# Kernel optimization log

Measured on AMD Instinct MI355X. Metric: run time of the kernel, lower is better.

The kernel has to match this reference:

```python
import jax, jax.numpy as jnp
import numpy as np

HEADS, DK, DV = 8, 64, 64
DM = HEADS * DK                 # 512
ROUNDS, SEQ, BUCKET = 2, 4096, 64
NCHUNK = SEQ // BUCKET          # 64 chunks
NBUCKETS = SEQ // BUCKET        # 64 hash buckets (Reformer convention)
SCALE = 8.0                     # sqrt(d_k)
NEG_BIG = -1e15
BATCH = 4


def setup_inputs() -> dict:
    key = jax.random.key(0)
    kq, kk, kv, kr = jax.random.split(key, 4)
    q = jax.random.normal(kq, (BATCH, SEQ, DM), jnp.float32)
    k = jax.random.normal(kk, (BATCH, SEQ, DM), jnp.float32)
    v = jax.random.normal(kv, (BATCH, SEQ, DM), jnp.float32)
    # angular-LSH random rotations: (rounds, d_model, n_buckets//2)
    R = jax.random.normal(kr, (ROUNDS, DM, NBUCKETS // 2), jnp.float32)
    return {"q": q, "k": k, "v": v, "R": R}


def _window(x):
    # x: (r, b, S, ...) -> (r, b, n_chunks, 2*BUCKET, ...)
    # each window = [previous chunk (wrapped), current chunk]
    r, b, S = x.shape[:3]
    xc = x.reshape((r, b, NCHUNK, BUCKET) + x.shape[3:])
    return jnp.concatenate([jnp.roll(xc, 1, axis=2), xc], axis=3)


def _lsh_attention(q, k, v, R):
    b = q.shape[0]
    # --- hash queries (same sorted_idx reused for q, k, v, as in the module) ---
    rot = jnp.einsum('bsd,rdm->rbsm', q, R)                       # (r,b,S,nb/2)
    h = jnp.argmax(jnp.concatenate([rot, -rot], axis=-1), axis=-1)
    h = h.astype(jnp.int32) + 1                                    # bucket 0 reserved for padding
    sorted_idx = jnp.argsort(h, axis=-1, stable=True)              # (r,b,S)

    def gather(x):  # (b,S,d) -> (r,b,S,d) sorted by bucket per round
        xb = jnp.broadcast_to(x[None], (ROUNDS,) + x.shape)
        return jnp.take_along_axis(xb, sorted_idx[..., None], axis=2)

    qs, ks, vs = gather(q), gather(k), gather(v)
    hs = jnp.take_along_axis(h, sorted_idx, axis=2)                # (r,b,S)

    # --- chunk into local windows ---
    qs = _window(qs.reshape(ROUNDS, b, SEQ, HEADS, DK))            # (r,b,n,2c,h,dk)
    ks = _window(ks.reshape(ROUNDS, b, SEQ, HEADS, DK))
    vs = _window(vs.reshape(ROUNDS, b, SEQ, HEADS, DV))
    hw = _window(hs)                                               # (r,b,n,2c)

    # --- per-window attention with bucket mask + log-count bias ---
    attn = jnp.einsum('rbnqhd,rbnkhd->rbnhqk', qs, ks) / SCALE     # (r,b,n,h,2c,2c)
    hm = (hw[:, :, :, :, None] == hw[:, :, :, None, :]) & (hw[:, :, :, :, None] != 0)
    hm = hm[:, :, :, None].astype(jnp.float32)                     # (r,b,n,1,2c,2c)
    cnt = hm * jnp.sum(hm, axis=4, keepdims=True)                  # count term (sum over q dim, as in source)
    bias = (1.0 - hm) * NEG_BIG - jnp.log(jnp.clip(cnt, 1.0))
    attn = attn + bias
    attn = attn + jnp.eye(2 * BUCKET, dtype=attn.dtype) * -1e5     # self-attention mask
    attn = jax.nn.softmax(attn, axis=-1)
    out = jnp.einsum('rbnhml,rbnlhd->rbnmhd', attn, vs)            # (r,b,n,2c,h,dv)
    out = out[:, :, :, BUCKET:]                                    # keep current-chunk queries
    out = out.reshape(ROUNDS, b, SEQ, HEADS, DV)

    # --- unsort back to original token order, sum over rounds ---
    inv = jnp.argsort(sorted_idx, axis=-1, stable=True)
    out = jnp.take_along_axis(out, inv[:, :, :, None, None], axis=2)
    return jnp.sum(out, axis=0)                                    # (b,S,heads,dv)


def reference(q, k, v, R):
    return _lsh_attention(q, k, v, R)
```

## Files before the change

### kernel.cpp

```cpp
#include <hip/hip_runtime.h>
#include <hip/hip_bf16.h>
#include <hip/hip_fp16.h>

#define HEADS 8
#define DK 64
#define DV 64
#define DM 512
#define ROUNDS 2
#define SEQ 4096
#define BUCKET 64
#define NCHUNK 64
#define BATCH 4
#define GAP_THRESH 0.02f

typedef _Float16 f16;
typedef f16 f16x4 __attribute__((ext_vector_type(4)));
typedef f16 f16x8 __attribute__((ext_vector_type(8)));
typedef float f32x4 __attribute__((ext_vector_type(4)));

#define MFMA16(a, b, c) __builtin_amdgcn_mfma_f32_16x16x32_f16((a), (b), (c), 0, 0, 0)

__global__ __launch_bounds__(256) void hash_approx_kernel(
    const float* __restrict__ q, const float* __restrict__ R,
    int* __restrict__ h_out, unsigned char* __restrict__ flag) {
  int blk = blockIdx.x;
  int stile = blk & 63;
  int b = (blk >> 6) & (BATCH - 1);
  int r = blk >> 8;
  int s0 = stile << 6;
  int rb = r * BATCH + b;

  __shared__ f16 Rh[32 * 520];
  __shared__ f16 Rl[32 * 520];

  int tid = threadIdx.x;
  int w = tid >> 6, lane = tid & 63, lo = lane & 15, hi = lane >> 4;

  const float* rbase = R + (size_t)r * DM * 32;
#pragma unroll
  for (int i = 0; i < 16; ++i) {
    int fi = tid + i * 256;
    float4 rv = *reinterpret_cast<const float4*>(rbase + fi * 4);
    int d = fi >> 3, m0 = (fi & 7) * 4;
    const float* rp = &rv.x;
#pragma unroll
    for (int e = 0; e < 4; ++e) {
      float x = rp[e];
      f16 hx = (f16)x;
      Rh[(m0 + e) * 520 + d] = hx;
      Rl[(m0 + e) * 520 + d] = (f16)(x - (float)hx);
    }
  }
  __syncthreads();

  int qr = w * 16 + lo;
  const float* qp = q + ((size_t)b * SEQ + s0 + qr) * DM;

  f32x4 acc0 = {0.f, 0.f, 0.f, 0.f}, acc1 = {0.f, 0.f, 0.f, 0.f};
#pragma unroll 4
  for (int ks = 0; ks < 16; ++ks) {
    int k = ks * 32 + hi * 8;
    float4 a0 = *reinterpret_cast<const float4*>(qp + k);
    float4 a1 = *reinterpret_cast<const float4*>(qp + k + 4);
    float av[8] = {a0.x, a0.y, a0.z, a0.w, a1.x, a1.y, a1.z, a1.w};
    f16x8 ahi, alo;
#pragma unroll
    for (int e = 0; e < 8; ++e) {
      f16 hx = (f16)av[e];
      ahi[e] = hx;
      alo[e] = (f16)(av[e] - (float)hx);
    }
    f16x8 bh0 = *reinterpret_cast<const f16x8*>(&Rh[lo * 520 + k]);
    f16x8 bl0 = *reinterpret_cast<const f16x8*>(&Rl[lo * 520 + k]);
    f16x8 bh1 = *reinterpret_cast<const f16x8*>(&Rh[(16 + lo) * 520 + k]);
    f16x8 bl1 = *reinterpret_cast<const f16x8*>(&Rl[(16 + lo) * 520 + k]);
    acc0 = MFMA16(ahi, bh0, acc0);
    acc0 = MFMA16(ahi, bl0, acc0);
    acc0 = MFMA16(alo, bh0, acc0);
    acc1 = MFMA16(ahi, bh1, acc1);
    acc1 = MFMA16(ahi, bl1, acc1);
    acc1 = MFMA16(alo, bh1, acc1);
  }

#pragma unroll
  for (int rg = 0; rg < 4; ++rg) {
    float c0 = acc0[rg], c1 = acc1[rg];
    float v1 = c0;
    int i1 = lo;
    float v2 = -INFINITY;
    float cv[3] = {c1, -c0, -c1};
    int ci[3] = {16 + lo, 32 + lo, 48 + lo};
#pragma unroll
    for (int c = 0; c < 3; ++c) {
      if (cv[c] > v1) { v2 = v1; v1 = cv[c]; i1 = ci[c]; }
      else v2 = fmaxf(v2, cv[c]);
    }
#pragma unroll
    for (int off = 1; off <= 8; off <<= 1) {
      float ov1 = __shfl_xor(v1, off);
      int oi1 = __shfl_xor(i1, off);
      float ov2 = __shfl_xor(v2, off);
      if (ov1 > v1 || (ov1 == v1 && oi1 < i1)) {
        v2 = fmaxf(v1, ov2);
        v1 = ov1;
        i1 = oi1;
      } else {
        v2 = fmaxf(v2, ov1);
      }
    }
    if (lo == 0) {
      int grow = s0 + w * 16 + hi * 4 + rg;
      size_t gid = (size_t)rb * SEQ + grow;
      h_out[gid] = i1 + 1;
      flag[gid] = (v1 - v2 <= GAP_THRESH) ? 1 : 0;
    }
  }
}

__global__ __launch_bounds__(256) void hash_exact_kernel(
    const float* __restrict__ q, const float* __restrict__ R,
    const unsigned char* __restrict__ flag, int* __restrict__ h_out) {
  int g0 = blockIdx.x * 64;
  __shared__ int nf;
  __shared__ unsigned char list[64];
  __shared__ double pl[8][33];
  int tid = threadIdx.x;
  if (tid == 0) nf = 0;
  __syncthreads();
  if (tid < 64 && flag[g0 + tid]) {
    int idx = atomicAdd(&nf, 1);
    list[idx] = (unsigned char)tid;
  }
  __syncthreads();
  int n = nf;
  for (int i = 0; i < n; ++i) {
    int g = g0 + list[i];
    int rb = g >> 12, s = g & (SEQ - 1);
    int r = rb >> 2, b = rb & (BATCH - 1);
    int m = tid & 31, chunk = tid >> 5;
    const float* qp = q + ((size_t)b * SEQ + s) * DM;
    const float* rp = R + (size_t)r * DM * 32;
    double part = 0.0;
    for (int dd = 0; dd < 64; ++dd) {
      int d = chunk * 64 + dd;
      part = fma((double)qp[d], (double)rp[(size_t)d * 32 + m], part);
    }
    pl[chunk][m] = part;
    __syncthreads();
    if (tid < 32) {
      double sum = 0.0;
#pragma unroll
      for (int c = 0; c < 8; ++c) sum += pl[c][m];
      double v = sum;
      int ix = m;
      double nv = -sum;
      if (nv > v) { v = nv; ix = m + 32; }
      for (int off = 1; off <= 16; off <<= 1) {
        double ov = __shfl_xor(v, off);
        int oi = __shfl_xor(ix, off);
        if (ov > v || (ov == v && oi < ix)) { v = ov; ix = oi; }
      }
      if (tid == 0) h_out[g] = ix + 1;
    }
    __syncthreads();
  }
}

__global__ __launch_bounds__(256) void sort_kernel(const int* __restrict__ h,
                                                   int* __restrict__ sorted_idx) {
  int rb = blockIdx.x;
  const int* hp = h + (size_t)rb * SEQ;
  __shared__ unsigned char hs[SEQ];
  __shared__ unsigned char rs[SEQ];
  __shared__ int tile_cnt[64][64];
  __shared__ int tile_base[64][64];
  __shared__ int bucket_base[64];
  __shared__ int bucket_tot[64];
  int tid = threadIdx.x;
  int wave = tid >> 6, lane = tid & 63;
  for (int i = tid; i < 64 * 64; i += 256) ((int*)tile_cnt)[i] = 0;
  __syncthreads();
  for (int t = wave; t < 64; t += 4) {
    int s = (t << 6) + lane;
    int hv = hp[s] - 1;
    unsigned long long mm = ~0ull;
#pragma unroll
    for (int bit = 0; bit < 6; ++bit) {
      unsigned long long bb = __ballot((hv >> bit) & 1);
      mm &= ((hv >> bit) & 1) ? bb : ~bb;
    }
    int rank = __popcll(mm & ((1ull << lane) - 1ull));
    hs[s] = (unsigned char)hv;
    rs[s] = (unsigned char)rank;
    if (rank == 0) tile_cnt[t][hv] = __popcll(mm);
  }
  __syncthreads();
  if (tid < 64) {
    int bkt = tid;
    int run = 0;
    for (int t = 0; t < 64; ++t) { tile_base[t][bkt] = run; run += tile_cnt[t][bkt]; }
    bucket_tot[bkt] = run;
  }
  __syncthreads();
  if (tid == 0) {
    int run = 0;
    for (int bkt = 0; bkt < 64; ++bkt) { bucket_base[bkt] = run; run += bucket_tot[bkt]; }
  }
  __syncthreads();
  for (int t = wave; t < 64; t += 4) {
    int s = (t << 6) + lane;
    int hv = hs[s];
    int pos = bucket_base[hv] + tile_base[t][hv] + rs[s];
    sorted_idx[(size_t)rb * SEQ + pos] = s;
  }
}

__global__ __launch_bounds__(256, 4) void attn_kernel(
    const float* __restrict__ q, const float* __restrict__ k,
    const float* __restrict__ v, const int* __restrict__ h,
    const int* __restrict__ sidx, float* __restrict__ out) {
  int x = blockIdx.x;
  int hd = x & 7;
  int n = (x >> 3) & 63;
  int b = (x >> 9) & (BATCH - 1);
  int r = x >> 11;
  int rb = r * BATCH + b;

  __shared__ __align__(16) unsigned char smem[34816];
  __shared__ int orig_w[128];
  __shared__ int hw[128];
  f16* Qh = reinterpret_cast<f16*>(smem);
  f16* Kh = reinterpret_cast<f16*>(smem + 9216);
  const int VOFF = 17408;

  int tid = threadIdx.x;
  int wave = tid >> 6;
  int lane = tid & 63;
  int lo = lane & 15;
  int hi = lane >> 4;

  if (tid < 128) {
    int j = tid;
    int sp = (j < 64) ? ((((n + 63) & 63) << 6) + j) : ((n << 6) + (j - 64));
    int orig = sidx[(size_t)rb * SEQ + sp];
    orig_w[j] = orig;
    hw[j] = h[(size_t)rb * SEQ + orig];
  }
  __syncthreads();

  const size_t gbase = (size_t)b * SEQ * DM + hd * 64;

  float4 kreg[8], qreg[4];
#pragma unroll
  for (int t = 0; t < 8; ++t) {
    int idx = tid + t * 256;
    int j = idx >> 4, dq = idx & 15;
    kreg[t] = *reinterpret_cast<const float4*>(
        k + gbase + (size_t)orig_w[j] * DM + dq * 4);
  }
#pragma unroll
  for (int t = 0; t < 4; ++t) {
    int idx = tid + t * 256;
    int i = idx >> 4, dq = idx & 15;
    qreg[t] = *reinterpret_cast<const float4*>(
        q + gbase + (size_t)orig_w[64 + i] * DM + dq * 4);
  }
#pragma unroll
  for (int t = 0; t < 8; ++t) {
    int idx = tid + t * 256;
    int j = idx >> 4, dq = idx & 15;
    f16x4 hv = {(f16)kreg[t].x, (f16)kreg[t].y, (f16)kreg[t].z, (f16)kreg[t].w};
    *reinterpret_cast<f16x4*>(&Kh[j * 72 + dq * 4]) = hv;
  }
#pragma unroll
  for (int t = 0; t < 4; ++t) {
    int idx = tid + t * 256;
    int i = idx >> 4, dq = idx & 15;
    f16x4 hv = {(f16)qreg[t].x, (f16)qreg[t].y, (f16)qreg[t].z, (f16)qreg[t].w};
    *reinterpret_cast<f16x4*>(&Qh[i * 72 + dq * 4]) = hv;
  }
  __syncthreads();

  float4 vreg[8];
#pragma unroll
  for (int t = 0; t < 8; ++t) {
    int idx = tid + t * 256;
    int l = idx >> 4, dq = idx & 15;
    vreg[t] = *reinterpret_cast<const float4*>(
        v + gbase + (size_t)orig_w[l] * DM + dq * 4);
  }

  f32x4 acc[8];
#pragma unroll
  for (int t = 0; t < 8; ++t) acc[t] = (f32x4){0.f, 0.f, 0.f, 0.f};

  int qr_a = wave * 16 + lo;
  f16x8 aq0 = *reinterpret_cast<const f16x8*>(&Qh[qr_a * 72 + hi * 8]);
  f16x8 aq1 = *reinterpret_cast<const f16x8*>(&Qh[qr_a * 72 + 32 + hi * 8]);
#pragma unroll
  for (int t = 0; t < 8; ++t) {
    f16x8 b0 = *reinterpret_cast<const f16x8*>(&Kh[(t * 16 + lo) * 72 + hi * 8]);
    f16x8 b1 = *reinterpret_cast<const f16x8*>(&Kh[(t * 16 + lo) * 72 + 32 + hi * 8]);
    acc[t] = MFMA16(aq0, b0, acc[t]);
    acc[t] = MFMA16(aq1, b1, acc[t]);
  }

  int hq[4];
#pragma unroll
  for (int rg = 0; rg < 4; ++rg) hq[rg] = hw[64 + wave * 16 + hi * 4 + rg];
#pragma unroll
  for (int t = 0; t < 8; ++t) {
    int key = t * 16 + lo;
    int hj = hw[key];
#pragma unroll
    for (int rg = 0; rg < 4; ++rg) {
      int qr = wave * 16 + hi * 4 + rg;
      float lg = acc[t][rg] * 0.125f;
      if (hj != hq[rg]) lg = -1e15f;
      if (key == 64 + qr) lg -= 1e5f;
      acc[t][rg] = lg;
    }
  }
  float mx[4] = {-INFINITY, -INFINITY, -INFINITY, -INFINITY};
#pragma unroll
  for (int t = 0; t < 8; ++t)
#pragma unroll
    for (int rg = 0; rg < 4; ++rg) mx[rg] = fmaxf(mx[rg], acc[t][rg]);
#pragma unroll
  for (int off = 1; off <= 8; off <<= 1)
#pragma unroll
    for (int rg = 0; rg < 4; ++rg) mx[rg] = fmaxf(mx[rg], __shfl_xor(mx[rg], off));
  float sm[4] = {0.f, 0.f, 0.f, 0.f};
#pragma unroll
  for (int t = 0; t < 8; ++t)
#pragma unroll
    for (int rg = 0; rg < 4; ++rg) {
      float ev = __expf(acc[t][rg] - mx[rg]);
      acc[t][rg] = ev;
      sm[rg] += ev;
    }
#pragma unroll
  for (int off = 1; off <= 8; off <<= 1)
#pragma unroll
    for (int rg = 0; rg < 4; ++rg) sm[rg] += __shfl_xor(sm[rg], off);
  float inv[4];
#pragma unroll
  for (int rg = 0; rg < 4; ++rg) inv[rg] = 1.0f / sm[rg];

  __syncthreads();

#pragma unroll
  for (int t = 0; t < 8; ++t) {
    int key = t * 16 + lo;
#pragma unroll
    for (int rg = 0; rg < 4; ++rg) {
      int qr = wave * 16 + hi * 4 + rg;
      *reinterpret_cast<f16*>(smem + qr * 272 + key * 2) =
          (f16)(acc[t][rg] * inv[rg]);
    }
  }
#pragma unroll
  for (int t = 0; t < 8; ++t) {
    int idx = tid + t * 256;
    int l = idx >> 4, dq = idx & 15;
    const float* vp = &vreg[t].x;
#pragma unroll
    for (int c = 0; c < 4; ++c) {
      int dv = dq * 4 + c;
      int off = (l * 2 + (((dv >> 3) & 7) << 4)) & 255;
      *reinterpret_cast<f16*>(smem + VOFF + dv * 272 + off) = (f16)vp[c];
    }
  }
  __syncthreads();

  f32x4 o[4];
#pragma unroll
  for (int dt = 0; dt < 4; ++dt) o[dt] = (f32x4){0.f, 0.f, 0.f, 0.f};
#pragma unroll
  for (int lt = 0; lt < 4; ++lt) {
    f16x8 ap = *reinterpret_cast<const f16x8*>(
        smem + qr_a * 272 + lt * 64 + hi * 16);
#pragma unroll
    for (int dt = 0; dt < 4; ++dt) {
      int dvr = dt * 16 + lo;
      int off = (lt * 64 + hi * 16 + (((dvr >> 3) & 7) << 4)) & 255;
      f16x8 bv = *reinterpret_cast<const f16x8*>(smem + VOFF + dvr * 272 + off);
      o[dt] = MFMA16(ap, bv, o[dt]);
    }
  }

#pragma unroll
  for (int dt = 0; dt < 4; ++dt) {
#pragma unroll
    for (int rg = 0; rg < 4; ++rg) {
      int qr = wave * 16 + hi * 4 + rg;
      float* dst = out + gbase + (size_t)orig_w[64 + qr] * DM + dt * 16 + lo;
      atomicAdd(dst, o[dt][rg]);
    }
  }
}

extern "C" void kernel_launch(void* const* d_in, const int* in_sizes, int n_in,
                              void* d_out, int out_size, void* d_ws,
                              size_t ws_size, hipStream_t stream) {
  (void)out_size; (void)ws_size;
  const int R_ELEMS = ROUNDS * DM * 32;
  const float *q, *k, *v, *R;
  if (n_in >= 4 && in_sizes[0] == R_ELEMS) {
    R = (const float*)d_in[0];
    k = (const float*)d_in[1];
    q = (const float*)d_in[2];
    v = (const float*)d_in[3];
  } else {
    q = (const float*)d_in[0];
    k = (const float*)d_in[1];
    v = (const float*)d_in[2];
    R = (const float*)d_in[3];
  }
  float* out = (float*)d_out;
  char* ws = (char*)d_ws;
  int* h = (int*)ws;
  int* sidx = (int*)(ws + ROUNDS * BATCH * SEQ * 4);
  unsigned char* flag = (unsigned char*)(ws + 2 * ROUNDS * BATCH * SEQ * 4);

  hipMemsetAsync(out, 0, (size_t)BATCH * SEQ * DM * sizeof(float), stream);
  hash_approx_kernel<<<ROUNDS * BATCH * (SEQ / 64), 256, 0, stream>>>(q, R, h, flag);
  hash_exact_kernel<<<ROUNDS * BATCH * (SEQ / 64), 256, 0, stream>>>(q, R, flag, h);
  sort_kernel<<<ROUNDS * BATCH, 256, 0, stream>>>(h, sidx);
  attn_kernel<<<ROUNDS * BATCH * NCHUNK * HEADS, 256, 0, stream>>>(q, k, v, h, sidx, out);
}
```

Baseline: 217.9 us.

## Keep softmax probabilities in registers via transposed MFMA and cut LDS footprint

The attention kernel now computes S^T with swapped MFMA operands, so each lane owns a single query row, and the row-wise softmax reductions shrink to two cross-lane shuffles. Probabilities are packed to f16 and redistributed with wave shuffles straight into the B operand of the PV MFMA, so the P tile and the Q staging buffer no longer live in LDS. Q is loaded directly from global memory into registers. LDS per block drops from about 34KB to 18KB and the launch bound asks for 8 blocks per CU, aiming at higher occupancy. The cost is many more shuffle instructions, a chance of register pressure under the tighter launch bound, and uncoalesced per-lane Q loads.

```diff
diff --git a/kernel.cpp b/kernel.cpp
--- a/kernel.cpp
+++ b/kernel.cpp
@@ -19,6 +19,13 @@
 typedef float f32x4 __attribute__((ext_vector_type(4)));
 
 #define MFMA16(a, b, c) __builtin_amdgcn_mfma_f32_16x16x32_f16((a), (b), (c), 0, 0, 0)
+
+__device__ __forceinline__ unsigned int pk2(float a, float b) {
+  union { f16 h[2]; unsigned int u; } c;
+  c.h[0] = (f16)a;
+  c.h[1] = (f16)b;
+  return c.u;
+}
 
 __global__ __launch_bounds__(256) void hash_approx_kernel(
     const float* __restrict__ q, const float* __restrict__ R,
@@ -215,7 +222,7 @@
   }
 }
 
-__global__ __launch_bounds__(256, 4) void attn_kernel(
+__global__ __launch_bounds__(256, 8) void attn_kernel(
     const float* __restrict__ q, const float* __restrict__ k,
     const float* __restrict__ v, const int* __restrict__ h,
     const int* __restrict__ sidx, float* __restrict__ out) {
@@ -226,12 +233,10 @@
   int r = x >> 11;
   int rb = r * BATCH + b;
 
-  __shared__ __align__(16) unsigned char smem[34816];
+  __shared__ __align__(16) unsigned char smem[18432];
   __shared__ int orig_w[128];
   __shared__ int hw[128];
-  f16* Qh = reinterpret_cast<f16*>(smem);
-  f16* Kh = reinterpret_cast<f16*>(smem + 9216);
-  const int VOFF = 17408;
+  f16* Kh = reinterpret_cast<f16*>(smem);
 
   int tid = threadIdx.x;
   int wave = tid >> 6;
@@ -250,125 +255,132 @@
 
   const size_t gbase = (size_t)b * SEQ * DM + hd * 64;
 
-  float4 kreg[8], qreg[4];
-#pragma unroll
-  for (int t = 0; t < 8; ++t) {
-    int idx = tid + t * 256;
-    int j = idx >> 4, dq = idx & 15;
-    kreg[t] = *reinterpret_cast<const float4*>(
-        k + gbase + (size_t)orig_w[j] * DM + dq * 4);
-  }
-#pragma unroll
-  for (int t = 0; t < 4; ++t) {
-    int idx = tid + t * 256;
-    int i = idx >> 4, dq = idx & 15;
-    qreg[t] = *reinterpret_cast<const float4*>(
-        q + gbase + (size_t)orig_w[64 + i] * DM + dq * 4);
-  }
-#pragma unroll
-  for (int t = 0; t < 8; ++t) {
-    int idx = tid + t * 256;
-    int j = idx >> 4, dq = idx & 15;
-    f16x4 hv = {(f16)kreg[t].x, (f16)kreg[t].y, (f16)kreg[t].z, (f16)kreg[t].w};
-    *reinterpret_cast<f16x4*>(&Kh[j * 72 + dq * 4]) = hv;
-  }
-#pragma unroll
-  for (int t = 0; t < 4; ++t) {
-    int idx = tid + t * 256;
-    int i = idx >> 4, dq = idx & 15;
-    f16x4 hv = {(f16)qreg[t].x, (f16)qreg[t].y, (f16)qreg[t].z, (f16)qreg[t].w};
-    *reinterpret_cast<f16x4*>(&Qh[i * 72 + dq * 4]) = hv;
-  }
-  __syncthreads();
-
-  float4 vreg[8];
-#pragma unroll
-  for (int t = 0; t < 8; ++t) {
-    int idx = tid + t * 256;
-    int l = idx >> 4, dq = idx & 15;
-    vreg[t] = *reinterpret_cast<const float4*>(
-        v + gbase + (size_t)orig_w[l] * DM + dq * 4);
+  {
+    float4 kreg[8];
+#pragma unroll
+    for (int t = 0; t < 8; ++t) {
+      int idx = tid + t * 256;
+      int j = idx >> 4, dq = idx & 15;
+      kreg[t] = *reinterpret_cast<const float4*>(
+          k + gbase + (size_t)orig_w[j] * DM + dq * 4);
+    }
+#pragma unroll
+    for (int t = 0; t < 8; ++t) {
+      int idx = tid + t * 256;
+      int j = idx >> 4, dq = idx & 15;
+      f16x4 hv4 = {(f16)kreg[t].x, (f16)kreg[t].y, (f16)kreg[t].z, (f16)kreg[t].w};
+      *reinterpret_cast<f16x4*>(&Kh[j * 72 + dq * 4]) = hv4;
+    }
+  }
+  __syncthreads();
+
+  int qrow = wave * 16 + lo;
+  int qorig = orig_w[64 + qrow];
+  const float* qp = q + gbase + (size_t)qorig * DM;
+  f16x8 aq0, aq1;
+  {
+    float4 qa = *reinterpret_cast<const float4*>(qp + hi * 8);
+    float4 qb = *reinterpret_cast<const float4*>(qp + hi * 8 + 4);
+    float4 qc = *reinterpret_cast<const float4*>(qp + 32 + hi * 8);
+    float4 qd = *reinterpret_cast<const float4*>(qp + 32 + hi * 8 + 4);
+    aq0[0] = (f16)qa.x; aq0[1] = (f16)qa.y; aq0[2] = (f16)qa.z; aq0[3] = (f16)qa.w;
+    aq0[4] = (f16)qb.x; aq0[5] = (f16)qb.y; aq0[6] = (f16)qb.z; aq0[7] = (f16)qb.w;
+    aq1[0] = (f16)qc.x; aq1[1] = (f16)qc.y; aq1[2] = (f16)qc.z; aq1[3] = (f16)qc.w;
+    aq1[4] = (f16)qd.x; aq1[5] = (f16)qd.y; aq1[6] = (f16)qd.z; aq1[7] = (f16)qd.w;
   }
 
   f32x4 acc[8];
 #pragma unroll
   for (int t = 0; t < 8; ++t) acc[t] = (f32x4){0.f, 0.f, 0.f, 0.f};
-
-  int qr_a = wave * 16 + lo;
-  f16x8 aq0 = *reinterpret_cast<const f16x8*>(&Qh[qr_a * 72 + hi * 8]);
-  f16x8 aq1 = *reinterpret_cast<const f16x8*>(&Qh[qr_a * 72 + 32 + hi * 8]);
 #pragma unroll
   for (int t = 0; t < 8; ++t) {
     f16x8 b0 = *reinterpret_cast<const f16x8*>(&Kh[(t * 16 + lo) * 72 + hi * 8]);
     f16x8 b1 = *reinterpret_cast<const f16x8*>(&Kh[(t * 16 + lo) * 72 + 32 + hi * 8]);
-    acc[t] = MFMA16(aq0, b0, acc[t]);
-    acc[t] = MFMA16(aq1, b1, acc[t]);
-  }
-
-  int hq[4];
-#pragma unroll
-  for (int rg = 0; rg < 4; ++rg) hq[rg] = hw[64 + wave * 16 + hi * 4 + rg];
+    acc[t] = MFMA16(b0, aq0, acc[t]);
+    acc[t] = MFMA16(b1, aq1, acc[t]);
+  }
+
+  int hq = hw[64 + qrow];
 #pragma unroll
   for (int t = 0; t < 8; ++t) {
-    int key = t * 16 + lo;
-    int hj = hw[key];
 #pragma unroll
     for (int rg = 0; rg < 4; ++rg) {
-      int qr = wave * 16 + hi * 4 + rg;
+      int key = t * 16 + hi * 4 + rg;
       float lg = acc[t][rg] * 0.125f;
-      if (hj != hq[rg]) lg = -1e15f;
-      if (key == 64 + qr) lg -= 1e5f;
+      if (hw[key] != hq) lg = -1e15f;
+      if (key == 64 + qrow) lg -= 1e5f;
       acc[t][rg] = lg;
     }
   }
-  float mx[4] = {-INFINITY, -INFINITY, -INFINITY, -INFINITY};
+
+  float mx = -INFINITY;
 #pragma unroll
   for (int t = 0; t < 8; ++t)
 #pragma unroll
-    for (int rg = 0; rg < 4; ++rg) mx[rg] = fmaxf(mx[rg], acc[t][rg]);
-#pragma unroll
-  for (int off = 1; off <= 8; off <<= 1)
-#pragma unroll
-    for (int rg = 0; rg < 4; ++rg) mx[rg] = fmaxf(mx[rg], __shfl_xor(mx[rg], off));
-  float sm[4] = {0.f, 0.f, 0.f, 0.f};
+    for (int rg = 0; rg < 4; ++rg) mx = fmaxf(mx, acc[t][rg]);
+  mx = fmaxf(mx, __shfl_xor(mx, 16));
+  mx = fmaxf(mx, __shfl_xor(mx, 32));
+  float sm = 0.f;
 #pragma unroll
   for (int t = 0; t < 8; ++t)
 #pragma unroll
     for (int rg = 0; rg < 4; ++rg) {
-      float ev = __expf(acc[t][rg] - mx[rg]);
+      float ev = __expf(acc[t][rg] - mx);
       acc[t][rg] = ev;
-      sm[rg] += ev;
-    }
-#pragma unroll
-  for (int off = 1; off <= 8; off <<= 1)
-#pragma unroll
-    for (int rg = 0; rg < 4; ++rg) sm[rg] += __shfl_xor(sm[rg], off);
-  float inv[4];
-#pragma unroll
-  for (int rg = 0; rg < 4; ++rg) inv[rg] = 1.0f / sm[rg];
-
-  __syncthreads();
-
+      sm += ev;
+    }
+  sm += __shfl_xor(sm, 16);
+  sm += __shfl_xor(sm, 32);
+  float inv = 1.0f / sm;
+
+  unsigned int pku[8][2];
 #pragma unroll
   for (int t = 0; t < 8; ++t) {
-    int key = t * 16 + lo;
-#pragma unroll
-    for (int rg = 0; rg < 4; ++rg) {
-      int qr = wave * 16 + hi * 4 + rg;
-      *reinterpret_cast<f16*>(smem + qr * 272 + key * 2) =
-          (f16)(acc[t][rg] * inv[rg]);
-    }
-  }
-#pragma unroll
-  for (int t = 0; t < 8; ++t) {
-    int idx = tid + t * 256;
-    int l = idx >> 4, dq = idx & 15;
-    const float* vp = &vreg[t].x;
-#pragma unroll
-    for (int c = 0; c < 4; ++c) {
-      int dv = dq * 4 + c;
-      int off = (l * 2 + (((dv >> 3) & 7) << 4)) & 255;
-      *reinterpret_cast<f16*>(smem + VOFF + dv * 272 + off) = (f16)vp[c];
+    pku[t][0] = pk2(acc[t][0] * inv, acc[t][1] * inv);
+    pku[t][1] = pk2(acc[t][2] * inv, acc[t][3] * inv);
+  }
+  int srcA = lo + ((hi & 1) << 5);
+  int srcB = srcA + 16;
+  int th = hi >> 1;
+  unsigned int pbw[4][4];
+#pragma unroll
+  for (int lt = 0; lt < 4; ++lt) {
+    unsigned int eA0 = (unsigned)__shfl((int)pku[2 * lt][0], srcA);
+    unsigned int eA1 = (unsigned)__shfl((int)pku[2 * lt][1], srcA);
+    unsigned int fA0 = (unsigned)__shfl((int)pku[2 * lt + 1][0], srcA);
+    unsigned int fA1 = (unsigned)__shfl((int)pku[2 * lt + 1][1], srcA);
+    unsigned int eB0 = (unsigned)__shfl((int)pku[2 * lt][0], srcB);
+    unsigned int eB1 = (unsigned)__shfl((int)pku[2 * lt][1], srcB);
+    unsigned int fB0 = (unsigned)__shfl((int)pku[2 * lt + 1][0], srcB);
+    unsigned int fB1 = (unsigned)__shfl((int)pku[2 * lt + 1][1], srcB);
+    pbw[lt][0] = th ? fA0 : eA0;
+    pbw[lt][1] = th ? fA1 : eA1;
+    pbw[lt][2] = th ? fB0 : eB0;
+    pbw[lt][3] = th ? fB1 : eB1;
+  }
+
+  __syncthreads();
+
+  {
+    float4 vreg[8];
+#pragma unroll
+    for (int t = 0; t < 8; ++t) {
+      int idx = tid + t * 256;
+      int l = idx >> 4, dq = idx & 15;
+      vreg[t] = *reinterpret_cast<const float4*>(
+          v + gbase + (size_t)orig_w[l] * DM + dq * 4);
+    }
+#pragma unroll
+    for (int t = 0; t < 8; ++t) {
+      int idx = tid + t * 256;
+      int l = idx >> 4, dq = idx & 15;
+      const float* vp = &vreg[t].x;
+#pragma unroll
+      for (int c = 0; c < 4; ++c) {
+        int dv = dq * 4 + c;
+        int off = (l * 2 + (((dv >> 3) & 7) << 4)) & 255;
+        *reinterpret_cast<f16*>(smem + dv * 272 + off) = (f16)vp[c];
+      }
     }
   }
   __syncthreads();
@@ -378,24 +390,27 @@
   for (int dt = 0; dt < 4; ++dt) o[dt] = (f32x4){0.f, 0.f, 0.f, 0.f};
 #pragma unroll
   for (int lt = 0; lt < 4; ++lt) {
-    f16x8 ap = *reinterpret_cast<const f16x8*>(
-        smem + qr_a * 272 + lt * 64 + hi * 16);
+    union { unsigned int u[4]; f16x8 v8; } pc;
+    pc.u[0] = pbw[lt][0];
+    pc.u[1] = pbw[lt][1];
+    pc.u[2] = pbw[lt][2];
+    pc.u[3] = pbw[lt][3];
+    f16x8 pb = pc.v8;
 #pragma unroll
     for (int dt = 0; dt < 4; ++dt) {
       int dvr = dt * 16 + lo;
       int off = (lt * 64 + hi * 16 + (((dvr >> 3) & 7) << 4)) & 255;
-      f16x8 bv = *reinterpret_cast<const f16x8*>(smem + VOFF + dvr * 272 + off);
-      o[dt] = MFMA16(ap, bv, o[dt]);
-    }
-  }
-
+      f16x8 av = *reinterpret_cast<const f16x8*>(smem + dvr * 272 + off);
+      o[dt] = MFMA16(av, pb, o[dt]);
+    }
+  }
+
+  float* rowp = out + gbase + (size_t)qorig * DM;
 #pragma unroll
   for (int dt = 0; dt < 4; ++dt) {
 #pragma unroll
     for (int rg = 0; rg < 4; ++rg) {
-      int qr = wave * 16 + hi * 4 + rg;
-      float* dst = out + gbase + (size_t)orig_w[64 + qr] * DM + dt * 16 + lo;
-      atomicAdd(dst, o[dt][rg]);
+      atomicAdd(rowp + dt * 16 + hi * 4 + rg, o[dt][rg]);
     }
   }
 }
```

Measured after the change: 392.9 us. 1.8x slower.
